# Kernel optimization log

Hardware: AMD Instinct MI355X
Metric: run time of the kernel (lower is better)

The kernel has to match this reference:

```python
import jax, jax.numpy as jnp
import numpy as np

B, S, E, H = 2, 2048, 1024, 16
Dh = E // H  # 64
KEEP = 0.9   # 1 - dropout_p
INV_SCALE = 1.0  # forward() default; call site does not pass inv_scale


def setup_inputs() -> dict:
    key = jax.random.key(0)
    ks = jax.random.split(key, 12)
    query = jax.random.normal(ks[0], (B, S, E), dtype=jnp.float32)
    key_t = jax.random.normal(ks[1], (B, S, E), dtype=jnp.float32)
    value = jax.random.normal(ks[2], (B, S, E), dtype=jnp.float32)
    attn_mask = jax.random.randint(ks[3], (B, S), 0, 2, dtype=jnp.int32)
    # pre-scaled inverted dropout keep-mask (deterministic stand-in for F.dropout)
    dropout_mask = (jax.random.uniform(ks[4], (B, H, S, S)) < KEEP).astype(jnp.float32) / KEEP
    Wq = jax.random.normal(ks[5], (E, E), dtype=jnp.float32) * 0.02
    bq = jnp.zeros((E,), dtype=jnp.float32)
    Wk = jax.random.normal(ks[6], (E, E), dtype=jnp.float32) * 0.02
    bk = jnp.zeros((E,), dtype=jnp.float32)
    Wv = jax.random.normal(ks[7], (E, E), dtype=jnp.float32) * 0.02
    bv = jnp.zeros((E,), dtype=jnp.float32)
    return {"query": query, "key": key_t, "value": value, "attn_mask": attn_mask,
            "dropout_mask": dropout_mask, "Wq": Wq, "bq": bq, "Wk": Wk, "bk": bk,
            "Wv": Wv, "bv": bv}


def _heads(x, W, b):
    # Linear then split heads: (B,S,E) -> (B,H,S,Dh)
    y = x @ W.T + b
    return y.reshape(B, S, H, Dh).transpose(0, 2, 1, 3)


def reference(query, key, value, attn_mask, dropout_mask, Wq, bq, Wk, bk, Wv, bv):
    q = _heads(query, Wq, bq)
    k = _heads(key, Wk, bk)
    v = _heads(value, Wv, bv)
    scores = jnp.einsum("bhqd,bhkd->bhqk", q, k) / INV_SCALE
    pad = (attn_mask == 0)[:, None, None, :]  # (B,1,1,S) True = masked
    scores = jnp.where(pad, -jnp.inf, scores)
    attn = jax.nn.softmax(scores, axis=-1) * dropout_mask
    out = jnp.einsum("bhqk,bhkd->bhqd", attn, v)  # (B,H,S,Dh)
    return out
```

## Files before the change

### kernel.cpp

```cpp
#include <hip/hip_runtime.h>

#define B_ 2
#define S_ 2048
#define E_ 1024
#define H_ 16
#define DH 64
#define MM (B_*S_)
#define BHN (B_*H_)

typedef unsigned short u16;
typedef unsigned int u32;
typedef __attribute__((ext_vector_type(8))) __bf16 bf16x8;
typedef __attribute__((ext_vector_type(4))) float f32x4;
typedef __attribute__((ext_vector_type(8))) u16 u16x8;
typedef __attribute__((ext_vector_type(4))) u16 u16x4;

static __device__ __forceinline__ u16 f2bf(float f) {
  u32 u = __builtin_bit_cast(u32, f);
  u += 0x7fffu + ((u >> 16) & 1u);
  return (u16)(u >> 16);
}
static __device__ __forceinline__ float bf2f(u16 h) {
  return __builtin_bit_cast(float, (u32)h << 16);
}
static __device__ __forceinline__ u32 sw(u32 byte) {
  return byte ^ (((byte >> 7) & 7u) << 4);
}
static __device__ __forceinline__ bf16x8 frag(const u16* lds, u32 byte) {
  return *(const bf16x8*)((const char*)lds + byte);
}
static __device__ __forceinline__ f32x4 mfma16(bf16x8 a, bf16x8 b, f32x4 c) {
  return __builtin_amdgcn_mfma_f32_16x16x32_bf16(a, b, c, 0, 0, 0);
}
static __device__ __forceinline__ void gload_lds16(const u16* g, u16* lds_base) {
  __builtin_amdgcn_global_load_lds(
      (const __attribute__((address_space(1))) u32*)g,
      (__attribute__((address_space(3))) u32*)lds_base, 16, 0, 0);
}

#define L2E 1.44269504088896340736f

struct SplitArg { const float* s; u16* h; u16* l; int n4; };

__global__ void split6_kernel(SplitArg a0, SplitArg a1, SplitArg a2,
                              SplitArg a3, SplitArg a4, SplitArg a5) {
  SplitArg A = (blockIdx.z == 0) ? a0 : (blockIdx.z == 1) ? a1 : (blockIdx.z == 2) ? a2
             : (blockIdx.z == 3) ? a3 : (blockIdx.z == 4) ? a4 : a5;
  int i = blockIdx.x * blockDim.x + threadIdx.x;
  int stride = gridDim.x * blockDim.x;
  if (A.l) {
    for (; i < A.n4; i += stride) {
      float4 v = ((const float4*)A.s)[i];
      u16x4 h, l;
      h.x = f2bf(v.x); l.x = f2bf(v.x - bf2f(h.x));
      h.y = f2bf(v.y); l.y = f2bf(v.y - bf2f(h.y));
      h.z = f2bf(v.z); l.z = f2bf(v.z - bf2f(h.z));
      h.w = f2bf(v.w); l.w = f2bf(v.w - bf2f(h.w));
      ((u16x4*)A.h)[i] = h;
      ((u16x4*)A.l)[i] = l;
    }
  } else {
    for (; i < A.n4; i += stride) {
      float4 v = ((const float4*)A.s)[i];
      u16x4 h;
      h.x = f2bf(v.x); h.y = f2bf(v.y); h.z = f2bf(v.z); h.w = f2bf(v.w);
      ((u16x4*)A.h)[i] = h;
    }
  }
}

__global__ void pack_mask(const int* __restrict__ am, u32* __restrict__ pm) {
  int w = threadIdx.x;
  if (w < 128) {
    int base = (w >> 6) * 2048 + (w & 63) * 32;
    u32 bits = 0;
#pragma unroll
    for (int j = 0; j < 8; ++j) {
      int4 v = *(const int4*)(am + base + j * 4);
      bits |= (v.x ? 1u : 0u) << (4 * j) | (v.y ? 1u : 0u) << (4 * j + 1) |
              (v.z ? 1u : 0u) << (4 * j + 2) | (v.w ? 1u : 0u) << (4 * j + 3);
    }
    pm[w] = bits;
  }
}

struct ProjArgs {
  const u16* xhi; const u16* xlo; const u16* whi; const u16* wlo;
  const float* bias; u16* ohi; u16* olo; int mode;
};

__global__ __launch_bounds__(256, 3) void proj_gemm(ProjArgs a0, ProjArgs a1, ProjArgs a2) {
  ProjArgs A = (blockIdx.z == 0) ? a0 : (blockIdx.z == 1) ? a1 : a2;
  __shared__ u16 As[128 * 64];
  __shared__ u16 Bs[128 * 64];
  const int t = threadIdx.x;
  const int l = t & 63, wid = t >> 6;
  const int g = l >> 4, ln = l & 15;
  const int wm = wid >> 1, wn = wid & 1;
  int bid = blockIdx.y * 8 + blockIdx.x;
  int sid = (bid & 7) * 32 + (bid >> 3);
  const int m0 = (sid >> 3) * 128, e0 = (sid & 7) * 128;

  f32x4 acc[4][4] = {};
  const int nkt = (A.mode == 2) ? 32 : 48;

  for (int kt = 0; kt < nkt; ++kt) {
    int kp = kt * 64;
    const u16* asrc = (kp < 2048) ? A.xhi : A.xlo;
    const u16* bsrc = (kp < 1024 || kp >= 2048) ? A.whi : A.wlo;
    int kc = kp & 1023;
#pragma unroll
    for (int r = 0; r < 4; ++r) {
      int cr = wid * 4 + r;
      int row = cr * 8 + (l >> 3);
      int col = (l & 7) * 8;
      gload_lds16(asrc + (size_t)(m0 + row) * 1024 + kc + col, As + cr * 512);
      gload_lds16(bsrc + (size_t)(e0 + row) * 1024 + kc + col, Bs + cr * 512);
    }
    __syncthreads();
#pragma unroll
    for (int ks = 0; ks < 2; ++ks) {
      bf16x8 af[4], bfv[4];
#pragma unroll
      for (int i = 0; i < 4; ++i) {
        af[i] = frag(As, (u32)(wm * 64 + i * 16 + ln) * 128 + ks * 64 + g * 16);
        bfv[i] = frag(Bs, (u32)(wn * 64 + i * 16 + ln) * 128 + ks * 64 + g * 16);
      }
#pragma unroll
      for (int i = 0; i < 4; ++i)
#pragma unroll
        for (int j = 0; j < 4; ++j)
          acc[i][j] = mfma16(af[i], bfv[j], acc[i][j]);
    }
    __syncthreads();
  }

#pragma unroll
  for (int i = 0; i < 4; ++i) {
#pragma unroll
    for (int j = 0; j < 4; ++j) {
      int e = e0 + wn * 64 + j * 16 + ln;
      int h = e >> 6, d = e & 63;
      float bias = A.bias[e];
      if (A.mode < 2) {
#pragma unroll
        for (int r = 0; r < 4; ++r) {
          int m = m0 + wm * 64 + i * 16 + g * 4 + r;
          float v = acc[i][j][r] + bias;
          if (A.mode == 0) v *= L2E;
          int b = m >> 11, s = m & 2047;
          size_t idx = ((size_t)((b * 16 + h) * 2048 + s)) * 64 + d;
          u16 hv = f2bf(v);
          A.ohi[idx] = hv;
          A.olo[idx] = f2bf(v - bf2f(hv));
        }
      } else {
        int m = m0 + wm * 64 + i * 16 + g * 4;
        int b = m >> 11, s = m & 2047;
        u16x4 pv;
#pragma unroll
        for (int r = 0; r < 4; ++r) pv[r] = f2bf(acc[i][j][r] + bias);
        size_t idx = ((size_t)((b * 16 + h) * 64 + d)) * 2048 + s;
        *(u16x4*)(A.ohi + idx) = pv;
      }
    }
  }
}

__global__ __launch_bounds__(256, 3) void attn_kernel(
    const u16* __restrict__ qhi, const u16* __restrict__ qlo,
    const u16* __restrict__ khi, const u16* __restrict__ klo,
    const u16* __restrict__ vt, const u32* __restrict__ pm,
    const float* __restrict__ dmask, float* __restrict__ out) {
  __shared__ u16 Ksh[64 * 64];
  __shared__ u16 Ksl[64 * 64];
  __shared__ u16 Vs[64 * 64];
  __shared__ u16 Ps[4 * 16 * 64];

  const int t = threadIdx.x, l = t & 63, wid = t >> 6;
  const int g = l >> 4, ln = l & 15;

  int bid = blockIdx.y * 32 + blockIdx.x;
  int sid = (bid & 7) * 128 + (bid >> 3);
  const int qt = sid & 31, bh = sid >> 5, b = bh >> 4;
  const int q0 = qt * 64;
  const int qrow = q0 + wid * 16 + ln;
  const size_t qg = ((size_t)bh * 2048 + qrow) * 64;
  const u32* pmb = pm + b * 64;

  bf16x8 qh[2], ql[2];
#pragma unroll
  for (int ks = 0; ks < 2; ++ks) {
    qh[ks] = *(const bf16x8*)(qhi + qg + ks * 32 + g * 8);
    ql[ks] = *(const bf16x8*)(qlo + qg + ks * 32 + g * 8);
  }

  const size_t dmrow = ((size_t)bh * 2048 + qrow) * 2048;
  float4 dmc[4], dmn[4];
  auto load_dm = [&](int kt, float4* d) {
    const int k0 = kt * 64;
#pragma unroll
    for (int i = 0; i < 4; ++i)
      d[i] = *(const float4*)(dmask + dmrow + k0 + i * 16 + 4 * g);
  };

  u16x8 rkh[2], rkl[2], rv[2];
  auto load_tile = [&](int kt) {
    const int k0 = kt * 64;
    const size_t kbase = ((size_t)bh * 2048 + k0) * 64;
#pragma unroll
    for (int i = 0; i < 2; ++i) {
      int c = t + 256 * i;
      rkh[i] = *(const u16x8*)(khi + kbase + c * 8);
      rkl[i] = *(const u16x8*)(klo + kbase + c * 8);
      int row = c >> 3;
      rv[i] = *(const u16x8*)(vt + ((size_t)bh * 64 + row) * 2048 + k0 + (c & 7) * 8);
    }
  };
  auto write_tile = [&]() {
#pragma unroll
    for (int i = 0; i < 2; ++i) {
      int c = t + 256 * i;
      u32 lb = sw((u32)c * 16);
      *(u16x8*)((char*)Ksh + lb) = rkh[i];
      *(u16x8*)((char*)Ksl + lb) = rkl[i];
      *(u16x8*)((char*)Vs + lb) = rv[i];
    }
  };

  load_dm(0, dmc);
  load_tile(0);
  write_tile();
  __syncthreads();

  f32x4 O[4] = {};
  float Zacc = 0.f;
  const u32 psbase = (u32)(wid * 2048 + ln * 128);

  for (int kt = 0; kt < 32; ++kt) {
    if (kt < 31) {
      load_dm(kt + 1, dmn);
      load_tile(kt + 1);
    }
    u32 m0 = pmb[2 * kt], m1 = pmb[2 * kt + 1];

    f32x4 sc[4] = {};
#pragma unroll
    for (int ks = 0; ks < 2; ++ks) {
#pragma unroll
      for (int i = 0; i < 4; ++i) {
        u32 byt = sw((u32)((i * 16 + ln) * 128 + ks * 64 + g * 16));
        bf16x8 akh = frag(Ksh, byt);
        bf16x8 akl = frag(Ksl, byt);
        sc[i] = mfma16(akh, qh[ks], sc[i]);
        sc[i] = mfma16(akh, ql[ks], sc[i]);
        sc[i] = mfma16(akl, qh[ks], sc[i]);
      }
    }

#pragma unroll
    for (int i = 0; i < 4; ++i) {
      u32 mm = (i < 2 ? m0 : m1) >> (((i & 1) << 4) + 4 * g);
      float e0 = (mm & 1u) ? exp2f(sc[i][0]) : 0.f;
      float e1 = (mm & 2u) ? exp2f(sc[i][1]) : 0.f;
      float e2 = (mm & 4u) ? exp2f(sc[i][2]) : 0.f;
      float e3 = (mm & 8u) ? exp2f(sc[i][3]) : 0.f;
      Zacc += (e0 + e1) + (e2 + e3);
      u16x4 p;
      p.x = f2bf(e0 * dmc[i].x);
      p.y = f2bf(e1 * dmc[i].y);
      p.z = f2bf(e2 * dmc[i].z);
      p.w = f2bf(e3 * dmc[i].w);
      *(u16x4*)((char*)Ps + sw(psbase + i * 32 + g * 8)) = p;
    }

#pragma unroll
    for (int ks = 0; ks < 2; ++ks) {
      bf16x8 bP = frag(Ps, sw(psbase + ks * 64 + g * 16));
#pragma unroll
      for (int id = 0; id < 4; ++id) {
        bf16x8 aV = frag(Vs, sw((u32)((id * 16 + ln) * 128 + ks * 64 + g * 16)));
        O[id] = mfma16(aV, bP, O[id]);
      }
    }

    __syncthreads();
    if (kt < 31) {
      write_tile();
      __syncthreads();
#pragma unroll
      for (int i = 0; i < 4; ++i) dmc[i] = dmn[i];
    }
  }

  float z = Zacc;
  z += __shfl_xor(z, 16, 64);
  z += __shfl_xor(z, 32, 64);
  float rz = 1.f / z;

#pragma unroll
  for (int id = 0; id < 4; ++id) {
    float4 o;
    o.x = O[id][0] * rz; o.y = O[id][1] * rz;
    o.z = O[id][2] * rz; o.w = O[id][3] * rz;
    *(float4*)(out + qg + id * 16 + 4 * g) = o;
  }
}

extern "C" void kernel_launch(void* const* d_in, const int* in_sizes, int n_in,
                              void* d_out, int out_size, void* d_ws, size_t ws_size,
                              hipStream_t stream) {
  const float* query = (const float*)d_in[0];
  const float* keyt  = (const float*)d_in[1];
  const float* value = (const float*)d_in[2];
  const int*   amask = (const int*)d_in[3];
  const float* dmask = (const float*)d_in[4];
  const float* Wq = (const float*)d_in[5];
  const float* bq = (const float*)d_in[6];
  const float* Wk = (const float*)d_in[7];
  const float* bk = (const float*)d_in[8];
  const float* Wv = (const float*)d_in[9];
  const float* bv = (const float*)d_in[10];

  char* ws = (char*)d_ws;
  size_t off = 0;
  auto alloc = [&](size_t bytes) {
    char* p = ws + off;
    off += (bytes + 255) & ~(size_t)255;
    return p;
  };
  const size_t XB = (size_t)MM * E_ * sizeof(u16);
  const size_t WB = (size_t)E_ * E_ * sizeof(u16);

  u16 *xh[3], *xl[3], *wh[3], *wl[3];
  for (int i = 0; i < 3; ++i) { xh[i] = (u16*)alloc(XB); xl[i] = (u16*)alloc(XB); }
  for (int i = 0; i < 3; ++i) { wh[i] = (u16*)alloc(WB); wl[i] = (u16*)alloc(WB); }
  u16* q_hi = (u16*)alloc(XB);
  u16* q_lo = (u16*)alloc(XB);
  u16* k_hi = (u16*)alloc(XB);
  u16* k_lo = (u16*)alloc(XB);
  u16* v_t  = (u16*)alloc(XB);
  u32* pmask = (u32*)alloc(512);
  if (off > ws_size) return;

  SplitArg sa[6] = {
      {query, xh[0], xl[0], MM * E_ / 4}, {keyt, xh[1], xl[1], MM * E_ / 4},
      {value, xh[2], nullptr, MM * E_ / 4}, {Wq, wh[0], wl[0], E_ * E_ / 4},
      {Wk, wh[1], wl[1], E_ * E_ / 4},    {Wv, wh[2], wl[2], E_ * E_ / 4},
  };
  split6_kernel<<<dim3(512, 1, 6), 256, 0, stream>>>(sa[0], sa[1], sa[2], sa[3], sa[4], sa[5]);
  pack_mask<<<1, 128, 0, stream>>>(amask, pmask);

  ProjArgs pa[3] = {
      {xh[0], xl[0], wh[0], wl[0], bq, q_hi, q_lo, 0},
      {xh[1], xl[1], wh[1], wl[1], bk, k_hi, k_lo, 1},
      {xh[2], nullptr, wh[2], wl[2], bv, v_t, nullptr, 2},
  };
  proj_gemm<<<dim3(8, 32, 3), 256, 0, stream>>>(pa[0], pa[1], pa[2]);

  attn_kernel<<<dim3(32, 32), 256, 0, stream>>>(
      q_hi, q_lo, k_hi, k_lo, v_t, pmask, dmask, (float*)d_out);
}
```

Measured before the change: 294.7 us.

## Read K and V fragments directly from global memory instead of LDS tiles

Removes the shared-memory staging of K-hi, K-lo and V tiles in the attention kernel. Each wave now loads its MFMA operand fragments straight from global memory (relying on L1/L2 for reuse across the four waves), which drops two block-wide barriers per key tile and the LDS writes. In exchange, every wave issues its own global loads for the same data, there is no explicit software prefetch of K/V any more, and the loads sit on the critical path just before the MFMAs.

After: 527.5 us. 79.0% more time.

```diff
diff --git a/kernel.cpp b/kernel.cpp
--- a/kernel.cpp
+++ b/kernel.cpp
@@ -28,6 +28,9 @@
 }
 static __device__ __forceinline__ bf16x8 frag(const u16* lds, u32 byte) {
   return *(const bf16x8*)((const char*)lds + byte);
+}
+static __device__ __forceinline__ bf16x8 gfrag(const u16* g) {
+  return *(const bf16x8*)g;
 }
 static __device__ __forceinline__ f32x4 mfma16(bf16x8 a, bf16x8 b, f32x4 c) {
   return __builtin_amdgcn_mfma_f32_16x16x32_bf16(a, b, c, 0, 0, 0);
@@ -172,9 +175,6 @@
     const u16* __restrict__ khi, const u16* __restrict__ klo,
     const u16* __restrict__ vt, const u32* __restrict__ pm,
     const float* __restrict__ dmask, float* __restrict__ out) {
-  __shared__ u16 Ksh[64 * 64];
-  __shared__ u16 Ksl[64 * 64];
-  __shared__ u16 Vs[64 * 64];
   __shared__ u16 Ps[4 * 16 * 64];
 
   const int t = threadIdx.x, l = t & 63, wid = t >> 6;
@@ -204,44 +204,17 @@
       d[i] = *(const float4*)(dmask + dmrow + k0 + i * 16 + 4 * g);
   };
 
-  u16x8 rkh[2], rkl[2], rv[2];
-  auto load_tile = [&](int kt) {
-    const int k0 = kt * 64;
-    const size_t kbase = ((size_t)bh * 2048 + k0) * 64;
-#pragma unroll
-    for (int i = 0; i < 2; ++i) {
-      int c = t + 256 * i;
-      rkh[i] = *(const u16x8*)(khi + kbase + c * 8);
-      rkl[i] = *(const u16x8*)(klo + kbase + c * 8);
-      int row = c >> 3;
-      rv[i] = *(const u16x8*)(vt + ((size_t)bh * 64 + row) * 2048 + k0 + (c & 7) * 8);
-    }
-  };
-  auto write_tile = [&]() {
-#pragma unroll
-    for (int i = 0; i < 2; ++i) {
-      int c = t + 256 * i;
-      u32 lb = sw((u32)c * 16);
-      *(u16x8*)((char*)Ksh + lb) = rkh[i];
-      *(u16x8*)((char*)Ksl + lb) = rkl[i];
-      *(u16x8*)((char*)Vs + lb) = rv[i];
-    }
-  };
-
   load_dm(0, dmc);
-  load_tile(0);
-  write_tile();
-  __syncthreads();
 
   f32x4 O[4] = {};
   float Zacc = 0.f;
   const u32 psbase = (u32)(wid * 2048 + ln * 128);
+  const u32 kfo = (u32)(ln * 64 + g * 8);
+  const size_t vbase0 = ((size_t)bh * 64 + ln) * 2048 + g * 8;
 
   for (int kt = 0; kt < 32; ++kt) {
-    if (kt < 31) {
-      load_dm(kt + 1, dmn);
-      load_tile(kt + 1);
-    }
+    const size_t kbase = ((size_t)bh * 2048 + kt * 64) * 64;
+    if (kt < 31) load_dm(kt + 1, dmn);
     u32 m0 = pmb[2 * kt], m1 = pmb[2 * kt + 1];
 
     f32x4 sc[4] = {};
@@ -249,9 +222,9 @@
     for (int ks = 0; ks < 2; ++ks) {
 #pragma unroll
       for (int i = 0; i < 4; ++i) {
-        u32 byt = sw((u32)((i * 16 + ln) * 128 + ks * 64 + g * 16));
-        bf16x8 akh = frag(Ksh, byt);
-        bf16x8 akl = frag(Ksl, byt);
+        const size_t off = kbase + kfo + i * 1024 + ks * 32;
+        bf16x8 akh = gfrag(khi + off);
+        bf16x8 akl = gfrag(klo + off);
         sc[i] = mfma16(akh, qh[ks], sc[i]);
         sc[i] = mfma16(akh, ql[ks], sc[i]);
         sc[i] = mfma16(akl, qh[ks], sc[i]);
@@ -279,15 +252,12 @@
       bf16x8 bP = frag(Ps, sw(psbase + ks * 64 + g * 16));
 #pragma unroll
       for (int id = 0; id < 4; ++id) {
-        bf16x8 aV = frag(Vs, sw((u32)((id * 16 + ln) * 128 + ks * 64 + g * 16)));
+        bf16x8 aV = gfrag(vt + vbase0 + (size_t)id * 32768 + kt * 64 + ks * 32);
         O[id] = mfma16(aV, bP, O[id]);
       }
     }
 
-    __syncthreads();
     if (kt < 31) {
-      write_tile();
-      __syncthreads();
 #pragma unroll
       for (int i = 0; i < 4; ++i) dmc[i] = dmn[i];
     }
```
